# Kernel optimization log

Hardware: AMD Instinct MI355X
Metric: run time of the kernel (lower is better)

Reference implementation:

```python
import jax, jax.numpy as jnp
import numpy as np

# Static module configuration (matches init_kwargs)
H, W, C, K = 40, 40, 1, 5
HOUT, WOUT = H - K + 1, W - K + 1
P = HOUT * WOUT * C          # patch_count = 1296
L = K * K * C                # patch_length = 25
M = 384                      # num_inducing
N = 64                       # batch
JITTER = 1e-6


def extract_patches(X):
    """im2col: [N,H,W,C] -> [N, P, L], stride 1, VALID."""
    i = jnp.arange(HOUT)[:, None] + jnp.arange(K)[None, :]   # [HOUT,K]
    j = jnp.arange(WOUT)[:, None] + jnp.arange(K)[None, :]   # [WOUT,K]
    p = X[:, i, :, :]            # [N,HOUT,K,W,C]
    p = p[:, :, :, j, :]         # [N,HOUT,K,WOUT,K,C]
    p = jnp.transpose(p, (0, 1, 3, 2, 4, 5))  # [N,HOUT,WOUT,K,K,C]
    return p.reshape(X.shape[0], P, L)


def rbf(A, B, var, ls):
    """Isotropic RBF kernel K(A,B), A:[a,L], B:[b,L] -> [a,b]."""
    a2 = jnp.sum(A * A, -1)[:, None]
    b2 = jnp.sum(B * B, -1)[None, :]
    sq = jnp.maximum(a2 + b2 - 2.0 * (A @ B.T), 0.0)
    return var * jnp.exp(-0.5 * sq / (ls * ls))


def setup_inputs() -> dict:
    key = jax.random.key(0)
    k0, k1, k2, k3 = jax.random.split(key, 4)
    X = jax.random.normal(k0, (N, H * W * C), jnp.float32)
    Z = jax.random.normal(k1, (M, L), jnp.float32)
    q_mu = jax.random.normal(k2, (M, 1), jnp.float32)
    q_sqrt = jax.random.normal(k3, (M, M), jnp.float32) * 0.1
    variance = jnp.ones((1,), jnp.float32)
    lengthscale = jnp.ones((1,), jnp.float32) * 2.0
    return {"X": X, "Z": Z, "q_mu": q_mu, "q_sqrt": q_sqrt,
            "variance": variance, "lengthscale": lengthscale}


def reference(X, Z, q_mu, q_sqrt, variance, lengthscale):
    """conditional_ND with full_cov=False, white=False, Zero mean function.
    Returns (mean [N,P], var [N,P])."""
    var = variance[0]
    ls = lengthscale[0]
    n = X.shape[0]
    Ximg = X.reshape(n, H, W, C)
    patches = extract_patches(Ximg)                       # [N,P,L]

    # Kuf: M x (N*P) -- same as reshaping PMN_Kzx; solves act on M only
    Kuf = rbf(Z, patches.reshape(n * P, L), var, ls)       # [M, N*P]
    Kuu = rbf(Z, Z, var, ls) + JITTER * jnp.eye(M, dtype=X.dtype)
    Lu = jnp.linalg.cholesky(Kuu)

    # A = Kuu^{-1} Kuf via two triangular solves (white=False path)
    A = jax.scipy.linalg.solve_triangular(Lu, Kuf, lower=True)
    A = jax.scipy.linalg.solve_triangular(Lu.T, A, lower=False)
    A = A.reshape(M, n, P)                                 # [M,N,P]

    # mean = A^T q_mu per patch (q_mu shared across patches), + Zero mean fn
    mean = jnp.einsum('mnp,m->np', A, q_mu[:, 0])          # [N,P]

    # S - Kuu, shared across all P outputs
    Lq = jnp.tril(q_sqrt)
    SK = Lq @ Lq.T - Kuu                                   # [M,M]

    # diag of A^T (S - Kuu) A per (n,p)
    diag = jnp.einsum('mnp,mk,knp->np', A, SK, A)          # [N,P]

    # Kdiag of RBF kernel is the variance
    Kdiag = var * jnp.ones((n, P), X.dtype)
    return mean, Kdiag + diag
```

## Files before the change

kernel.cpp:

```cpp
#include <hip/hip_runtime.h>
#include <hip/hip_bf16.h>

#define HH 40
#define WW 40
#define KK 5
#define PP 1296
#define LL 25
#define MM 384
#define NN 64
#define NPTS (NN * PP)
#define JITTER 1e-6f

typedef unsigned short u16;
typedef unsigned int   u32;
using short8  = __attribute__((ext_vector_type(8))) short;
using floatx4 = __attribute__((ext_vector_type(4))) float;

#define FRAG_N (MM * MM)
#define ZFRAG_N (24 * 64 * 8)

__device__ inline u16 f2bf(float v) {
    u32 b = __float_as_uint(v);
    return (u16)((b + 0x7FFFu + ((b >> 16) & 1u)) >> 16);
}
__device__ inline float bf2f(u16 h) { return __uint_as_float(((u32)h) << 16); }
__device__ inline void split_bf16(float v, u16& hi, u16& lo) {
    hi = f2bf(v);
    lo = f2bf(v - bf2f(hi));
}

__device__ inline int frag_idx(int m, int k) {
    return (((m >> 4) * 12 + (k >> 5)) * 64 + ((m & 15) + (((k >> 3) & 3) << 4))) * 8 + (k & 7);
}

__device__ inline void frag_gemm64(const u16* __restrict__ Ah, const u16* __restrict__ Al,
                                   const u16* __restrict__ Bh, const u16* __restrict__ Bl,
                                   int bi, int bj, int w, int l, floatx4 acc[2][2]) {
    int mt0 = bi * 4 + 2 * (w & 1);
    int nt0 = bj * 4 + 2 * (w >> 1);
#pragma unroll
    for (int i = 0; i < 2; ++i)
#pragma unroll
        for (int jn = 0; jn < 2; ++jn) { floatx4 z = {0.f, 0.f, 0.f, 0.f}; acc[i][jn] = z; }
    for (int kt = 0; kt < 12; ++kt) {
        int ab0 = (((mt0 + 0) * 12 + kt) * 64 + l) * 8;
        int ab1 = (((mt0 + 1) * 12 + kt) * 64 + l) * 8;
        int bb0 = (((nt0 + 0) * 12 + kt) * 64 + l) * 8;
        int bb1 = (((nt0 + 1) * 12 + kt) * 64 + l) * 8;
        short8 a0h = *(const short8*)&Ah[ab0];
        short8 a0l = *(const short8*)&Al[ab0];
        short8 a1h = *(const short8*)&Ah[ab1];
        short8 a1l = *(const short8*)&Al[ab1];
        short8 b0h = *(const short8*)&Bh[bb0];
        short8 b0l = *(const short8*)&Bl[bb0];
        short8 b1h = *(const short8*)&Bh[bb1];
        short8 b1l = *(const short8*)&Bl[bb1];
        acc[0][0] = __builtin_amdgcn_mfma_f32_16x16x32_bf16(a0h, b0h, acc[0][0], 0, 0, 0);
        acc[0][0] = __builtin_amdgcn_mfma_f32_16x16x32_bf16(a0h, b0l, acc[0][0], 0, 0, 0);
        acc[0][0] = __builtin_amdgcn_mfma_f32_16x16x32_bf16(a0l, b0h, acc[0][0], 0, 0, 0);
        acc[0][1] = __builtin_amdgcn_mfma_f32_16x16x32_bf16(a0h, b1h, acc[0][1], 0, 0, 0);
        acc[0][1] = __builtin_amdgcn_mfma_f32_16x16x32_bf16(a0h, b1l, acc[0][1], 0, 0, 0);
        acc[0][1] = __builtin_amdgcn_mfma_f32_16x16x32_bf16(a0l, b1h, acc[0][1], 0, 0, 0);
        acc[1][0] = __builtin_amdgcn_mfma_f32_16x16x32_bf16(a1h, b0h, acc[1][0], 0, 0, 0);
        acc[1][0] = __builtin_amdgcn_mfma_f32_16x16x32_bf16(a1h, b0l, acc[1][0], 0, 0, 0);
        acc[1][0] = __builtin_amdgcn_mfma_f32_16x16x32_bf16(a1l, b0h, acc[1][0], 0, 0, 0);
        acc[1][1] = __builtin_amdgcn_mfma_f32_16x16x32_bf16(a1h, b1h, acc[1][1], 0, 0, 0);
        acc[1][1] = __builtin_amdgcn_mfma_f32_16x16x32_bf16(a1h, b1l, acc[1][1], 0, 0, 0);
        acc[1][1] = __builtin_amdgcn_mfma_f32_16x16x32_bf16(a1l, b1h, acc[1][1], 0, 0, 0);
    }
}

__device__ inline void dwrite_frag(u16* __restrict__ Oh, u16* __restrict__ Ol,
                                   int m, int p, float v) {
    int idx = frag_idx(m, p);
    u16 hi, lo;
    split_bf16(v, hi, lo);
    Oh[idx] = hi; Ol[idx] = lo;
}

__device__ inline void load_r0(const float* __restrict__ Kuu, float alpha,
                               int row, int kt, int l, short8& h8, short8& l8) {
    int kb = kt * 32 + ((l >> 4) << 3);
    const float* p = &Kuu[row * MM + kb];
    float4 f0 = *(const float4*)p;
    float4 f1 = *(const float4*)(p + 4);
    float vv[8] = {f0.x, f0.y, f0.z, f0.w, f1.x, f1.y, f1.z, f1.w};
#pragma unroll
    for (int j = 0; j < 8; ++j) {
        float r = ((row == kb + j) ? 1.f : 0.f) - alpha * vv[j];
        u16 h, lo;
        split_bf16(r, h, lo);
        h8[j] = (short)h; l8[j] = (short)lo;
    }
}

__global__ void __launch_bounds__(384) prep_kernel(
    const float* __restrict__ Z, const float* __restrict__ q_sqrt,
    const float* __restrict__ var_p, const float* __restrict__ ls_p,
    float* __restrict__ Kuu, float* __restrict__ rsum, float* __restrict__ z2g,
    u16* __restrict__ Qh, u16* __restrict__ Ql,
    u16* __restrict__ Zfh, u16* __restrict__ Zfl) {
    __shared__ float Zs[LL];
    __shared__ float red[384];
    int r = blockIdx.x, tid = threadIdx.x;
    if (tid < LL) Zs[tid] = Z[r * LL + tid];
    __syncthreads();
    float var = var_p[0];
    float ls = ls_p[0];
    float c0 = -0.5f / (ls * ls);
    float s = 0.f;
#pragma unroll
    for (int d = 0; d < LL; ++d) {
        float dd = Zs[d] - Z[tid * LL + d];
        s += dd * dd;
    }
    float v = var * expf(c0 * s);
    if (tid == r) v += JITTER;
    Kuu[r * MM + tid] = v;
    red[tid] = v;
    __syncthreads();
    if (tid < 128) red[tid] += red[tid + 256];
    __syncthreads();
    for (int o = 128; o > 0; o >>= 1) {
        if (tid < o) red[tid] += red[tid + o];
        __syncthreads();
    }
    if (tid == 0) {
        rsum[r] = red[0];
        float t = 0.f;
#pragma unroll
        for (int d = 0; d < LL; ++d) t += Zs[d] * Zs[d];
        z2g[r] = t;
    }
    {
        int o = r * MM + tid;
        int j = o & 7, ln = (o >> 3) & 63, kt = (o >> 9) % 12, mt = o / 6144;
        int m = mt * 16 + (ln & 15);
        int k = kt * 32 + ((ln >> 4) << 3) + j;
        float qv = (k <= m) ? q_sqrt[m * MM + k] : 0.f;
        u16 h, lo;
        split_bf16(qv, h, lo);
        Qh[o] = h; Ql[o] = lo;
        if (o < ZFRAG_N) {
            int zt = o >> 9;
            int mz = zt * 16 + (ln & 15);
            int kd = ((ln >> 4) << 3) + j;
            float zv = (kd < LL) ? Z[mz * LL + kd] : 0.f;
            split_bf16(zv, h, lo);
            Zfh[o] = h; Zfl[o] = lo;
        }
    }
}

__global__ void __launch_bounds__(256) ns1_kernel(
    const float* __restrict__ Kuu, const float* __restrict__ rsum,
    const u16* __restrict__ Qh, const u16* __restrict__ Ql,
    u16* __restrict__ Xh, u16* __restrict__ Xl,
    u16* __restrict__ Rh, u16* __restrict__ Rl,
    u16* __restrict__ SKh, u16* __restrict__ SKl) {
    __shared__ float red[256];
    int tid = threadIdx.x, blk = blockIdx.x;
    int w = tid >> 6, l = tid & 63;
    float alpha = 0.f;
    if (blk < 72) {
        float v0 = rsum[tid];
        if (tid < 128) v0 = fmaxf(v0, rsum[tid + 256]);
        red[tid] = v0;
        __syncthreads();
        for (int o = 128; o > 0; o >>= 1) {
            if (tid < o) red[tid] = fmaxf(red[tid], red[tid + o]);
            __syncthreads();
        }
        alpha = 1.0f / red[0];
    }
    if (blk < 36) {
        float a2 = alpha * alpha;
        for (int o = blk * 256 + tid; o < FRAG_N; o += 36 * 256) {
            int j = o & 7, ln = (o >> 3) & 63, kt = (o >> 9) % 12, mt = o / 6144;
            int m = mt * 16 + (ln & 15);
            int k = kt * 32 + ((ln >> 4) << 3) + j;
            float v = ((m == k) ? 2.f * alpha : 0.f) - a2 * Kuu[m * MM + k];
            u16 h, lo;
            split_bf16(v, h, lo);
            Xh[o] = h; Xl[o] = lo;
        }
    } else if (blk < 72) {
        int tile = blk - 36;
        int bi = tile / 6, bj = tile % 6;
        int mt0 = bi * 4 + 2 * (w & 1), nt0 = bj * 4 + 2 * (w >> 1);
        floatx4 acc[2][2];
#pragma unroll
        for (int i = 0; i < 2; ++i)
#pragma unroll
            for (int jn = 0; jn < 2; ++jn) { floatx4 z = {0.f,0.f,0.f,0.f}; acc[i][jn] = z; }
        for (int kt = 0; kt < 12; ++kt) {
            short8 a0h, a0l, a1h, a1l, b0h, b0l, b1h, b1l;
            load_r0(Kuu, alpha, (mt0 + 0) * 16 + (l & 15), kt, l, a0h, a0l);
            load_r0(Kuu, alpha, (mt0 + 1) * 16 + (l & 15), kt, l, a1h, a1l);
            load_r0(Kuu, alpha, (nt0 + 0) * 16 + (l & 15), kt, l, b0h, b0l);
            load_r0(Kuu, alpha, (nt0 + 1) * 16 + (l & 15), kt, l, b1h, b1l);
            acc[0][0] = __builtin_amdgcn_mfma_f32_16x16x32_bf16(a0h, b0h, acc[0][0], 0, 0, 0);
            acc[0][0] = __builtin_amdgcn_mfma_f32_16x16x32_bf16(a0h, b0l, acc[0][0], 0, 0, 0);
            acc[0][0] = __builtin_amdgcn_mfma_f32_16x16x32_bf16(a0l, b0h, acc[0][0], 0, 0, 0);
            acc[0][1] = __builtin_amdgcn_mfma_f32_16x16x32_bf16(a0h, b1h, acc[0][1], 0, 0, 0);
            acc[0][1] = __builtin_amdgcn_mfma_f32_16x16x32_bf16(a0h, b1l, acc[0][1], 0, 0, 0);
            acc[0][1] = __builtin_amdgcn_mfma_f32_16x16x32_bf16(a0l, b1h, acc[0][1], 0, 0, 0);
            acc[1][0] = __builtin_amdgcn_mfma_f32_16x16x32_bf16(a1h, b0h, acc[1][0], 0, 0, 0);
            acc[1][0] = __builtin_amdgcn_mfma_f32_16x16x32_bf16(a1h, b0l, acc[1][0], 0, 0, 0);
            acc[1][0] = __builtin_amdgcn_mfma_f32_16x16x32_bf16(a1l, b0h, acc[1][0], 0, 0, 0);
            acc[1][1] = __builtin_amdgcn_mfma_f32_16x16x32_bf16(a1h, b1h, acc[1][1], 0, 0, 0);
            acc[1][1] = __builtin_amdgcn_mfma_f32_16x16x32_bf16(a1h, b1l, acc[1][1], 0, 0, 0);
            acc[1][1] = __builtin_amdgcn_mfma_f32_16x16x32_bf16(a1l, b1h, acc[1][1], 0, 0, 0);
        }
#pragma unroll
        for (int i = 0; i < 2; ++i)
#pragma unroll
            for (int jn = 0; jn < 2; ++jn)
#pragma unroll
                for (int j = 0; j < 4; ++j) {
                    int m = (mt0 + i) * 16 + ((l >> 4) << 2) + j;
                    int p = (nt0 + jn) * 16 + (l & 15);
                    dwrite_frag(Rh, Rl, m, p, acc[i][jn][j]);
                }
    } else {
        int tile = blk - 72;
        int bi = tile / 6, bj = tile % 6;
        floatx4 acc[2][2];
        frag_gemm64(Qh, Ql, Qh, Ql, bi, bj, w, l, acc);
        int mt0 = bi * 4 + 2 * (w & 1), nt0 = bj * 4 + 2 * (w >> 1);
#pragma unroll
        for (int i = 0; i < 2; ++i)
#pragma unroll
            for (int jn = 0; jn < 2; ++jn)
#pragma unroll
                for (int j = 0; j < 4; ++j) {
                    int m = (mt0 + i) * 16 + ((l >> 4) << 2) + j;
                    int p = (nt0 + jn) * 16 + (l & 15);
                    dwrite_frag(SKh, SKl, m, p, acc[i][jn][j] - Kuu[m * MM + p]);
                }
    }
}

__global__ void __launch_bounds__(256) ns_kernel(
    const u16* __restrict__ cxh, const u16* __restrict__ cxl,
    const u16* __restrict__ crh, const u16* __restrict__ crl,
    u16* __restrict__ nxh, u16* __restrict__ nxl,
    u16* __restrict__ nrh, u16* __restrict__ nrl) {
    int blk = blockIdx.x, tid = threadIdx.x;
    bool isX = (blk < 36);
    int tile = isX ? blk : blk - 36;
    int bi = tile / 6, bj = tile % 6;
    int w = tid >> 6, l = tid & 63;
    floatx4 acc[2][2];
    frag_gemm64(isX ? cxh : crh, isX ? cxl : crl, crh, crl, bi, bj, w, l, acc);
    int mt0 = bi * 4 + 2 * (w & 1), nt0 = bj * 4 + 2 * (w >> 1);
    u16* Oh = isX ? nxh : nrh;
    u16* Ol = isX ? nxl : nrl;
#pragma unroll
    for (int i = 0; i < 2; ++i)
#pragma unroll
        for (int jn = 0; jn < 2; ++jn)
#pragma unroll
            for (int j = 0; j < 4; ++j) {
                int m = (mt0 + i) * 16 + ((l >> 4) << 2) + j;
                int p = (nt0 + jn) * 16 + (l & 15);
                float v = acc[i][jn][j];
                if (isX) {
                    int id = frag_idx(m, p);
                    v += bf2f(cxh[id]) + bf2f(cxl[id]);
                }
                dwrite_frag(Oh, Ol, m, p, v);
            }
}

__global__ void __launch_bounds__(256) y_kernel(
    const u16* __restrict__ Xh, const u16* __restrict__ Xl,
    const u16* __restrict__ SKh, const u16* __restrict__ SKl,
    const float* __restrict__ qmu,
    u16* __restrict__ Yh, u16* __restrict__ Yl, float* __restrict__ cvec) {
    __shared__ float q[MM];
    int tid = threadIdx.x, blk = blockIdx.x;
    int w = tid >> 6, l = tid & 63;
    if (blk < 36) {
        int bi = blk / 6, bj = blk % 6;
        floatx4 acc[2][2];
        frag_gemm64(Xh, Xl, SKh, SKl, bi, bj, w, l, acc);
        int mt0 = bi * 4 + 2 * (w & 1), nt0 = bj * 4 + 2 * (w >> 1);
#pragma unroll
        for (int i = 0; i < 2; ++i)
#pragma unroll
            for (int jn = 0; jn < 2; ++jn)
#pragma unroll
                for (int j = 0; j < 4; ++j) {
                    int m = (mt0 + i) * 16 + ((l >> 4) << 2) + j;
                    int p = (nt0 + jn) * 16 + (l & 15);
                    dwrite_frag(Yh, Yl, m, p, acc[i][jn][j]);
                }
    } else {
        if (tid < MM) q[tid] = qmu[tid];
        if (tid + 256 < MM) q[tid + 256] = qmu[tid + 256];
        __syncthreads();
        int mt = (blk - 36) * 4 + w;
        float s = 0.f;
        for (int kt = 0; kt < 12; ++kt) {
            int b = ((mt * 12 + kt) * 64 + l) * 8;
            short8 h8 = *(const short8*)&Xh[b];
            short8 l8 = *(const short8*)&Xl[b];
            int kb = kt * 32 + ((l >> 4) << 3);
#pragma unroll
            for (int j = 0; j < 8; ++j)
                s += (bf2f((u16)h8[j]) + bf2f((u16)l8[j])) * q[kb + j];
        }
        s += __shfl_xor(s, 16);
        s += __shfl_xor(s, 32);
        if (l < 16) cvec[mt * 16 + l] = s;
    }
}

__global__ void __launch_bounds__(256) bq_kernel(
    const u16* __restrict__ Yh, const u16* __restrict__ Yl,
    const u16* __restrict__ Xh, const u16* __restrict__ Xl,
    u16* __restrict__ Bh, u16* __restrict__ Bl) {
    int blk = blockIdx.x, tid = threadIdx.x;
    int bi = blk / 6, bj = blk % 6;
    int w = tid >> 6, l = tid & 63;
    floatx4 acc[2][2];
    frag_gemm64(Yh, Yl, Xh, Xl, bi, bj, w, l, acc);
    int mt0 = bi * 4 + 2 * (w & 1), nt0 = bj * 4 + 2 * (w >> 1);
#pragma unroll
    for (int i = 0; i < 2; ++i)
#pragma unroll
        for (int jn = 0; jn < 2; ++jn)
#pragma unroll
            for (int j = 0; j < 4; ++j) {
                int m = (mt0 + i) * 16 + ((l >> 4) << 2) + j;
                int p = (nt0 + jn) * 16 + (l & 15);
                dwrite_frag(Bh, Bl, m, p, acc[i][jn][j]);
            }
}

__global__ void __launch_bounds__(512) main_kernel(
    const float* __restrict__ Xin,
    const u16* __restrict__ Zfh, const u16* __restrict__ Zfl,
    const float* __restrict__ z2g,
    const u16* __restrict__ Bfh, const u16* __restrict__ Bfl,
    const float* __restrict__ cvec,
    const float* __restrict__ var_p, const float* __restrict__ ls_p,
    float* __restrict__ out) {
    __shared__ u16 kh[12 * 8 * 64 * 8];
    __shared__ float patch[128 * 36];
    __shared__ float zsq[MM];
    __shared__ float xsq[128];
    __shared__ float red[1024];

    int tid = threadIdx.x;
    int np0 = blockIdx.x * 128;
    float var = var_p[0];
    float ls = ls_p[0];
    float c2 = -0.72134752044f / (ls * ls);

    if (tid < MM) zsq[tid] = z2g[tid];
    for (int e = tid; e < 128 * 36; e += 512) {
        int pt = e / 36, c = e % 36;
        float v = 0.f;
        if (c < 25) {
            int np = np0 + pt;
            int n = np / PP, p = np % PP;
            int oi = p / 36, oj = p % 36;
            v = Xin[n * (HH * WW) + (oi + c / 5) * WW + (oj + c % 5)];
        }
        patch[e] = v;
    }
    __syncthreads();
    if (tid < 128) {
        float s = 0.f;
#pragma unroll
        for (int d = 0; d < LL; ++d) { float x = patch[tid * 36 + d]; s += x * x; }
        xsq[tid] = s;
    }
    __syncthreads();

    int w = tid >> 6, l = tid & 63;
    int u = l >> 4;

    u32 kpk[3][8][2];
    float mp[8] = {0.f, 0.f, 0.f, 0.f, 0.f, 0.f, 0.f, 0.f};

#pragma unroll
    for (int h = 0; h < 2; ++h) {
        short8 pbh[4], pbl[4];
#pragma unroll
        for (int nt = 0; nt < 4; ++nt) {
            int p = h * 64 + nt * 16 + (l & 15);
            int pb = p * 36 + (u << 3);
            float4 f0 = *(const float4*)&patch[pb];
            float4 f1 = *(const float4*)&patch[pb + 4];
            float xv[8] = {f0.x, f0.y, f0.z, f0.w, f1.x, f1.y, f1.z, f1.w};
#pragma unroll
            for (int j = 0; j < 8; ++j) {
                u16 hh, lo;
                split_bf16(xv[j], hh, lo);
                pbh[nt][j] = (short)hh;
                pbl[nt][j] = (short)lo;
            }
        }
        floatx4 acc2[3][4];
#pragma unroll
        for (int i = 0; i < 3; ++i) {
            int zt = w * 3 + i;
            short8 zah = *(const short8*)&Zfh[(zt * 64 + l) * 8];
            short8 zal = *(const short8*)&Zfl[(zt * 64 + l) * 8];
#pragma unroll
            for (int nt = 0; nt < 4; ++nt) {
                floatx4 z = {0.f, 0.f, 0.f, 0.f};
                z = __builtin_amdgcn_mfma_f32_16x16x32_bf16(zah, pbh[nt], z, 0, 0, 0);
                z = __builtin_amdgcn_mfma_f32_16x16x32_bf16(zah, pbl[nt], z, 0, 0, 0);
                z = __builtin_amdgcn_mfma_f32_16x16x32_bf16(zal, pbh[nt], z, 0, 0, 0);
                acc2[i][nt] = z;
            }
        }
#pragma unroll
        for (int i = 0; i < 3; ++i) {
            int a2 = w * 3 + i;
            int kt = a2 >> 1;
            int rr = 2 * (a2 & 1) + (u >> 1);
            int k0 = a2 * 16 + 4 * u;
            float4 c4 = *(const float4*)&cvec[k0];
            float cvl[4] = {c4.x, c4.y, c4.z, c4.w};
#pragma unroll
            for (int nt = 0; nt < 4; ++nt) {
                int ntg = h * 4 + nt;
                int p = h * 64 + nt * 16 + (l & 15);
                u16 hi[4];
#pragma unroll
                for (int j = 0; j < 4; ++j) {
                    float s = zsq[k0 + j] + xsq[p] - 2.f * acc2[i][nt][j];
                    float v = var * exp2f(s * c2);
                    mp[ntg] += cvl[j] * v;
                    hi[j] = f2bf(v);
                }
                u32 p0 = (u32)hi[0] | ((u32)hi[1] << 16);
                u32 p1 = (u32)hi[2] | ((u32)hi[3] << 16);
                int base = ((kt * 8 + ntg) * 64 + rr * 16 + (l & 15)) * 8 + 4 * (u & 1);
                *(u32*)&kh[base]     = p0;
                *(u32*)&kh[base + 2] = p1;
                kpk[i][ntg][0] = p0;
                kpk[i][ntg][1] = p1;
            }
        }
    }

#pragma unroll
    for (int nt = 0; nt < 8; ++nt) {
        mp[nt] += __shfl_xor(mp[nt], 16);
        mp[nt] += __shfl_xor(mp[nt], 32);
    }
    if (l < 16) {
#pragma unroll
        for (int nt = 0; nt < 8; ++nt) red[w * 128 + nt * 16 + l] = mp[nt];
    }
    __syncthreads();
    if (tid < 128) {
        float s = 0.f;
#pragma unroll
        for (int ww = 0; ww < 8; ++ww) s += red[ww * 128 + tid];
        out[np0 + tid] = s;
    }

    floatx4 acc[3][8];
#pragma unroll
    for (int i = 0; i < 3; ++i)
#pragma unroll
        for (int nt = 0; nt < 8; ++nt) { floatx4 z = {0.f, 0.f, 0.f, 0.f}; acc[i][nt] = z; }
    for (int kt = 0; kt < 12; ++kt) {
        short8 bh[8];
#pragma unroll
        for (int nt = 0; nt < 8; ++nt)
            bh[nt] = *(const short8*)&kh[((kt * 8 + nt) * 64 + l) * 8];
#pragma unroll
        for (int i = 0; i < 3; ++i) {
            int mt = w * 3 + i;
            int ab = ((mt * 12 + kt) * 64 + l) * 8;
            short8 ah = *(const short8*)&Bfh[ab];
            short8 al = *(const short8*)&Bfl[ab];
#pragma unroll
            for (int nt = 0; nt < 8; ++nt) {
                acc[i][nt] = __builtin_amdgcn_mfma_f32_16x16x32_bf16(ah, bh[nt], acc[i][nt], 0, 0, 0);
                acc[i][nt] = __builtin_amdgcn_mfma_f32_16x16x32_bf16(al, bh[nt], acc[i][nt], 0, 0, 0);
            }
        }
    }
    __syncthreads();

    float dp[8] = {0.f, 0.f, 0.f, 0.f, 0.f, 0.f, 0.f, 0.f};
#pragma unroll
    for (int i = 0; i < 3; ++i)
#pragma unroll
        for (int nt = 0; nt < 8; ++nt) {
            float kv0 = bf2f((u16)(kpk[i][nt][0] & 0xFFFFu));
            float kv1 = bf2f((u16)(kpk[i][nt][0] >> 16));
            float kv2 = bf2f((u16)(kpk[i][nt][1] & 0xFFFFu));
            float kv3 = bf2f((u16)(kpk[i][nt][1] >> 16));
            dp[nt] += kv0 * acc[i][nt][0] + kv1 * acc[i][nt][1]
                    + kv2 * acc[i][nt][2] + kv3 * acc[i][nt][3];
        }
#pragma unroll
    for (int nt = 0; nt < 8; ++nt) {
        dp[nt] += __shfl_xor(dp[nt], 16);
        dp[nt] += __shfl_xor(dp[nt], 32);
    }
    if (l < 16) {
#pragma unroll
        for (int nt = 0; nt < 8; ++nt) red[w * 128 + nt * 16 + l] = dp[nt];
    }
    __syncthreads();
    if (tid < 128) {
        float s = 0.f;
#pragma unroll
        for (int ww = 0; ww < 8; ++ww) s += red[ww * 128 + tid];
        out[NPTS + np0 + tid] = var + s;
    }
}

extern "C" void kernel_launch(void* const* d_in, const int* in_sizes, int n_in,
                              void* d_out, int out_size, void* d_ws, size_t ws_size,
                              hipStream_t stream) {
    const float* Xin    = (const float*)d_in[0];
    const float* Z      = (const float*)d_in[1];
    const float* q_mu   = (const float*)d_in[2];
    const float* q_sqrt = (const float*)d_in[3];
    const float* var_p  = (const float*)d_in[4];
    const float* ls_p   = (const float*)d_in[5];
    float* out = (float*)d_out;

    const size_t HB = (size_t)FRAG_N * 2;
    char* base = (char*)d_ws;
    float* Kuu = (float*)base;
    u16* Bqh = (u16*)base;
    u16* Bql = (u16*)(base + HB);
    u16* Xh_a = (u16*)(base + 2 * HB);
    u16* Xl_a = (u16*)(base + 3 * HB);
    u16* Xh_b = (u16*)(base + 4 * HB);
    u16* Xl_b = (u16*)(base + 5 * HB);
    u16* Rh_a = (u16*)(base + 6 * HB);
    u16* Rl_a = (u16*)(base + 7 * HB);
    u16* Rh_b = (u16*)(base + 8 * HB);
    u16* Rl_b = (u16*)(base + 9 * HB);
    u16* Qh   = (u16*)(base + 10 * HB);
    u16* Ql   = (u16*)(base + 11 * HB);
    u16* Yh = Qh;
    u16* Yl = Ql;
    u16* SKh  = (u16*)(base + 12 * HB);
    u16* SKl  = (u16*)(base + 13 * HB);
    char* pF = base + 14 * HB;
    u16* Zfh = (u16*)pF;
    u16* Zfl = (u16*)(pF + ZFRAG_N * 2);
    float* z2g  = (float*)(pF + ZFRAG_N * 4);
    float* cvec = z2g + MM;
    float* rsum = cvec + MM;

    prep_kernel<<<MM, 384, 0, stream>>>(Z, q_sqrt, var_p, ls_p, Kuu, rsum, z2g,
                                        Qh, Ql, Zfh, Zfl);
    ns1_kernel<<<108, 256, 0, stream>>>(Kuu, rsum, Qh, Ql,
                                        Xh_b, Xl_b, Rh_b, Rl_b, SKh, SKl);
    u16 *cxh = Xh_b, *cxl = Xl_b, *nxh = Xh_a, *nxl = Xl_a;
    u16 *crh = Rh_b, *crl = Rl_b, *nrh = Rh_a, *nrl = Rl_a;
    for (int it = 0; it < 5; ++it) {
        ns_kernel<<<72, 256, 0, stream>>>(cxh, cxl, crh, crl, nxh, nxl, nrh, nrl);
        u16* t;
        t = cxh; cxh = nxh; nxh = t;
        t = cxl; cxl = nxl; nxl = t;
        t = crh; crh = nrh; nrh = t;
        t = crl; crl = nrl; nrl = t;
    }
    y_kernel<<<42, 256, 0, stream>>>(cxh, cxl, SKh, SKl, q_mu, Yh, Yl, cvec);
    bq_kernel<<<36, 256, 0, stream>>>(Yh, Yl, cxh, cxl, Bqh, Bql);
    main_kernel<<<NPTS / 128, 512, 0, stream>>>(Xin, Zfh, Zfl, z2g, Bqh, Bql, cvec,
                                                var_p, ls_p, out);
}
```

Measured before the change: 197.2 us.

## Precompute Kuu fragments in prep and split main kernel into two interleaved halves

Prep now also writes Kuu in bf16 hi/lo fragment layout, computed directly from Z. ns1 can then run its R0 GEMM through the shared frag_gemm64 helper on K·K and apply the alpha-scaled identity terms in the epilogue, instead of converting Kuu on the fly. The main kernel is restructured so the B·K GEMM for the first 64 patches runs before the second half's kernel evaluation, with the mean reduction moved to the end. This is meant to overlap work and cut register pressure from holding 8 bh tiles at once, but it adds a __syncthreads, recomputes Kuu entries per element in prep (25-dim loop), and changes the rounding of the R0 algebra.

```diff
diff --git a/kernel.cpp b/kernel.cpp
--- a/kernel.cpp
+++ b/kernel.cpp
@@ -78,26 +78,11 @@
     Oh[idx] = hi; Ol[idx] = lo;
 }
 
-__device__ inline void load_r0(const float* __restrict__ Kuu, float alpha,
-                               int row, int kt, int l, short8& h8, short8& l8) {
-    int kb = kt * 32 + ((l >> 4) << 3);
-    const float* p = &Kuu[row * MM + kb];
-    float4 f0 = *(const float4*)p;
-    float4 f1 = *(const float4*)(p + 4);
-    float vv[8] = {f0.x, f0.y, f0.z, f0.w, f1.x, f1.y, f1.z, f1.w};
-#pragma unroll
-    for (int j = 0; j < 8; ++j) {
-        float r = ((row == kb + j) ? 1.f : 0.f) - alpha * vv[j];
-        u16 h, lo;
-        split_bf16(r, h, lo);
-        h8[j] = (short)h; l8[j] = (short)lo;
-    }
-}
-
 __global__ void __launch_bounds__(384) prep_kernel(
     const float* __restrict__ Z, const float* __restrict__ q_sqrt,
     const float* __restrict__ var_p, const float* __restrict__ ls_p,
     float* __restrict__ Kuu, float* __restrict__ rsum, float* __restrict__ z2g,
+    u16* __restrict__ Kfh, u16* __restrict__ Kfl,
     u16* __restrict__ Qh, u16* __restrict__ Ql,
     u16* __restrict__ Zfh, u16* __restrict__ Zfl) {
     __shared__ float Zs[LL];
@@ -137,10 +122,20 @@
         int j = o & 7, ln = (o >> 3) & 63, kt = (o >> 9) % 12, mt = o / 6144;
         int m = mt * 16 + (ln & 15);
         int k = kt * 32 + ((ln >> 4) << 3) + j;
+        u16 h, lo;
         float qv = (k <= m) ? q_sqrt[m * MM + k] : 0.f;
-        u16 h, lo;
         split_bf16(qv, h, lo);
         Qh[o] = h; Ql[o] = lo;
+        float s2 = 0.f;
+#pragma unroll
+        for (int d = 0; d < LL; ++d) {
+            float dd = Z[m * LL + d] - Z[k * LL + d];
+            s2 += dd * dd;
+        }
+        float kv = var * expf(c0 * s2);
+        if (m == k) kv += JITTER;
+        split_bf16(kv, h, lo);
+        Kfh[o] = h; Kfl[o] = lo;
         if (o < ZFRAG_N) {
             int zt = o >> 9;
             int mz = zt * 16 + (ln & 15);
@@ -154,6 +149,7 @@
 
 __global__ void __launch_bounds__(256) ns1_kernel(
     const float* __restrict__ Kuu, const float* __restrict__ rsum,
+    const u16* __restrict__ Kfh, const u16* __restrict__ Kfl,
     const u16* __restrict__ Qh, const u16* __restrict__ Ql,
     u16* __restrict__ Xh, u16* __restrict__ Xl,
     u16* __restrict__ Rh, u16* __restrict__ Rl,
@@ -187,31 +183,10 @@
     } else if (blk < 72) {
         int tile = blk - 36;
         int bi = tile / 6, bj = tile % 6;
+        floatx4 acc[2][2];
+        frag_gemm64(Kfh, Kfl, Kfh, Kfl, bi, bj, w, l, acc);
         int mt0 = bi * 4 + 2 * (w & 1), nt0 = bj * 4 + 2 * (w >> 1);
-        floatx4 acc[2][2];
-#pragma unroll
-        for (int i = 0; i < 2; ++i)
-#pragma unroll
-            for (int jn = 0; jn < 2; ++jn) { floatx4 z = {0.f,0.f,0.f,0.f}; acc[i][jn] = z; }
-        for (int kt = 0; kt < 12; ++kt) {
-            short8 a0h, a0l, a1h, a1l, b0h, b0l, b1h, b1l;
-            load_r0(Kuu, alpha, (mt0 + 0) * 16 + (l & 15), kt, l, a0h, a0l);
-            load_r0(Kuu, alpha, (mt0 + 1) * 16 + (l & 15), kt, l, a1h, a1l);
-            load_r0(Kuu, alpha, (nt0 + 0) * 16 + (l & 15), kt, l, b0h, b0l);
-            load_r0(Kuu, alpha, (nt0 + 1) * 16 + (l & 15), kt, l, b1h, b1l);
-            acc[0][0] = __builtin_amdgcn_mfma_f32_16x16x32_bf16(a0h, b0h, acc[0][0], 0, 0, 0);
-            acc[0][0] = __builtin_amdgcn_mfma_f32_16x16x32_bf16(a0h, b0l, acc[0][0], 0, 0, 0);
-            acc[0][0] = __builtin_amdgcn_mfma_f32_16x16x32_bf16(a0l, b0h, acc[0][0], 0, 0, 0);
-            acc[0][1] = __builtin_amdgcn_mfma_f32_16x16x32_bf16(a0h, b1h, acc[0][1], 0, 0, 0);
-            acc[0][1] = __builtin_amdgcn_mfma_f32_16x16x32_bf16(a0h, b1l, acc[0][1], 0, 0, 0);
-            acc[0][1] = __builtin_amdgcn_mfma_f32_16x16x32_bf16(a0l, b1h, acc[0][1], 0, 0, 0);
-            acc[1][0] = __builtin_amdgcn_mfma_f32_16x16x32_bf16(a1h, b0h, acc[1][0], 0, 0, 0);
-            acc[1][0] = __builtin_amdgcn_mfma_f32_16x16x32_bf16(a1h, b0l, acc[1][0], 0, 0, 0);
-            acc[1][0] = __builtin_amdgcn_mfma_f32_16x16x32_bf16(a1l, b0h, acc[1][0], 0, 0, 0);
-            acc[1][1] = __builtin_amdgcn_mfma_f32_16x16x32_bf16(a1h, b1h, acc[1][1], 0, 0, 0);
-            acc[1][1] = __builtin_amdgcn_mfma_f32_16x16x32_bf16(a1h, b1l, acc[1][1], 0, 0, 0);
-            acc[1][1] = __builtin_amdgcn_mfma_f32_16x16x32_bf16(a1l, b1h, acc[1][1], 0, 0, 0);
-        }
+        float a2 = alpha * alpha;
 #pragma unroll
         for (int i = 0; i < 2; ++i)
 #pragma unroll
@@ -220,7 +195,9 @@
                 for (int j = 0; j < 4; ++j) {
                     int m = (mt0 + i) * 16 + ((l >> 4) << 2) + j;
                     int p = (nt0 + jn) * 16 + (l & 15);
-                    dwrite_frag(Rh, Rl, m, p, acc[i][jn][j]);
+                    float v = a2 * acc[i][jn][j] - 2.f * alpha * Kuu[m * MM + p]
+                            + ((m == p) ? 1.f : 0.f);
+                    dwrite_frag(Rh, Rl, m, p, v);
                 }
     } else {
         int tile = blk - 72;
@@ -386,24 +363,23 @@
     u32 kpk[3][8][2];
     float mp[8] = {0.f, 0.f, 0.f, 0.f, 0.f, 0.f, 0.f, 0.f};
 
-#pragma unroll
-    for (int h = 0; h < 2; ++h) {
-        short8 pbh[4], pbl[4];
-#pragma unroll
-        for (int nt = 0; nt < 4; ++nt) {
-            int p = h * 64 + nt * 16 + (l & 15);
-            int pb = p * 36 + (u << 3);
-            float4 f0 = *(const float4*)&patch[pb];
-            float4 f1 = *(const float4*)&patch[pb + 4];
-            float xv[8] = {f0.x, f0.y, f0.z, f0.w, f1.x, f1.y, f1.z, f1.w};
-#pragma unroll
-            for (int j = 0; j < 8; ++j) {
-                u16 hh, lo;
-                split_bf16(xv[j], hh, lo);
-                pbh[nt][j] = (short)hh;
-                pbl[nt][j] = (short)lo;
-            }
-        }
+    short8 pb0h[4], pb0l[4];
+#pragma unroll
+    for (int nt = 0; nt < 4; ++nt) {
+        int p = nt * 16 + (l & 15);
+        int pb = p * 36 + (u << 3);
+        float4 f0 = *(const float4*)&patch[pb];
+        float4 f1 = *(const float4*)&patch[pb + 4];
+        float xv[8] = {f0.x, f0.y, f0.z, f0.w, f1.x, f1.y, f1.z, f1.w};
+#pragma unroll
+        for (int j = 0; j < 8; ++j) {
+            u16 hh, lo;
+            split_bf16(xv[j], hh, lo);
+            pb0h[nt][j] = (short)hh;
+            pb0l[nt][j] = (short)lo;
+        }
+    }
+    {
         floatx4 acc2[3][4];
 #pragma unroll
         for (int i = 0; i < 3; ++i) {
@@ -413,9 +389,9 @@
 #pragma unroll
             for (int nt = 0; nt < 4; ++nt) {
                 floatx4 z = {0.f, 0.f, 0.f, 0.f};
-                z = __builtin_amdgcn_mfma_f32_16x16x32_bf16(zah, pbh[nt], z, 0, 0, 0);
-                z = __builtin_amdgcn_mfma_f32_16x16x32_bf16(zah, pbl[nt], z, 0, 0, 0);
-                z = __builtin_amdgcn_mfma_f32_16x16x32_bf16(zal, pbh[nt], z, 0, 0, 0);
+                z = __builtin_amdgcn_mfma_f32_16x16x32_bf16(zah, pb0h[nt], z, 0, 0, 0);
+                z = __builtin_amdgcn_mfma_f32_16x16x32_bf16(zah, pb0l[nt], z, 0, 0, 0);
+                z = __builtin_amdgcn_mfma_f32_16x16x32_bf16(zal, pb0h[nt], z, 0, 0, 0);
                 acc2[i][nt] = z;
             }
         }
@@ -429,8 +405,96 @@
             float cvl[4] = {c4.x, c4.y, c4.z, c4.w};
 #pragma unroll
             for (int nt = 0; nt < 4; ++nt) {
-                int ntg = h * 4 + nt;
-                int p = h * 64 + nt * 16 + (l & 15);
+                int p = nt * 16 + (l & 15);
+                u16 hi[4];
+#pragma unroll
+                for (int j = 0; j < 4; ++j) {
+                    float s = zsq[k0 + j] + xsq[p] - 2.f * acc2[i][nt][j];
+                    float v = var * exp2f(s * c2);
+                    mp[nt] += cvl[j] * v;
+                    hi[j] = f2bf(v);
+                }
+                u32 p0 = (u32)hi[0] | ((u32)hi[1] << 16);
+                u32 p1 = (u32)hi[2] | ((u32)hi[3] << 16);
+                int base = ((kt * 8 + nt) * 64 + rr * 16 + (l & 15)) * 8 + 4 * (u & 1);
+                *(u32*)&kh[base]     = p0;
+                *(u32*)&kh[base + 2] = p1;
+                kpk[i][nt][0] = p0;
+                kpk[i][nt][1] = p1;
+            }
+        }
+    }
+    short8 pb1h[4], pb1l[4];
+#pragma unroll
+    for (int nt = 0; nt < 4; ++nt) {
+        int p = 64 + nt * 16 + (l & 15);
+        int pb = p * 36 + (u << 3);
+        float4 f0 = *(const float4*)&patch[pb];
+        float4 f1 = *(const float4*)&patch[pb + 4];
+        float xv[8] = {f0.x, f0.y, f0.z, f0.w, f1.x, f1.y, f1.z, f1.w};
+#pragma unroll
+        for (int j = 0; j < 8; ++j) {
+            u16 hh, lo;
+            split_bf16(xv[j], hh, lo);
+            pb1h[nt][j] = (short)hh;
+            pb1l[nt][j] = (short)lo;
+        }
+    }
+    __syncthreads();
+
+    floatx4 acc[3][8];
+#pragma unroll
+    for (int i = 0; i < 3; ++i)
+#pragma unroll
+        for (int nt = 0; nt < 8; ++nt) { floatx4 z = {0.f, 0.f, 0.f, 0.f}; acc[i][nt] = z; }
+
+    for (int kt = 0; kt < 12; ++kt) {
+        short8 bh[4];
+#pragma unroll
+        for (int nt = 0; nt < 4; ++nt)
+            bh[nt] = *(const short8*)&kh[((kt * 8 + nt) * 64 + l) * 8];
+#pragma unroll
+        for (int i = 0; i < 3; ++i) {
+            int mt = w * 3 + i;
+            int ab = ((mt * 12 + kt) * 64 + l) * 8;
+            short8 ah = *(const short8*)&Bfh[ab];
+            short8 al = *(const short8*)&Bfl[ab];
+#pragma unroll
+            for (int nt = 0; nt < 4; ++nt) {
+                acc[i][nt] = __builtin_amdgcn_mfma_f32_16x16x32_bf16(ah, bh[nt], acc[i][nt], 0, 0, 0);
+                acc[i][nt] = __builtin_amdgcn_mfma_f32_16x16x32_bf16(al, bh[nt], acc[i][nt], 0, 0, 0);
+            }
+        }
+    }
+
+    {
+        floatx4 acc2[3][4];
+#pragma unroll
+        for (int i = 0; i < 3; ++i) {
+            int zt = w * 3 + i;
+            short8 zah = *(const short8*)&Zfh[(zt * 64 + l) * 8];
+            short8 zal = *(const short8*)&Zfl[(zt * 64 + l) * 8];
+#pragma unroll
+            for (int nt = 0; nt < 4; ++nt) {
+                floatx4 z = {0.f, 0.f, 0.f, 0.f};
+                z = __builtin_amdgcn_mfma_f32_16x16x32_bf16(zah, pb1h[nt], z, 0, 0, 0);
+                z = __builtin_amdgcn_mfma_f32_16x16x32_bf16(zah, pb1l[nt], z, 0, 0, 0);
+                z = __builtin_amdgcn_mfma_f32_16x16x32_bf16(zal, pb1h[nt], z, 0, 0, 0);
+                acc2[i][nt] = z;
+            }
+        }
+#pragma unroll
+        for (int i = 0; i < 3; ++i) {
+            int a2 = w * 3 + i;
+            int kt = a2 >> 1;
+            int rr = 2 * (a2 & 1) + (u >> 1);
+            int k0 = a2 * 16 + 4 * u;
+            float4 c4 = *(const float4*)&cvec[k0];
+            float cvl[4] = {c4.x, c4.y, c4.z, c4.w};
+#pragma unroll
+            for (int nt = 0; nt < 4; ++nt) {
+                int ntg = 4 + nt;
+                int p = 64 + nt * 16 + (l & 15);
                 u16 hi[4];
 #pragma unroll
                 for (int j = 0; j < 4; ++j) {
@@ -449,34 +513,13 @@
             }
         }
     }
-
-#pragma unroll
-    for (int nt = 0; nt < 8; ++nt) {
-        mp[nt] += __shfl_xor(mp[nt], 16);
-        mp[nt] += __shfl_xor(mp[nt], 32);
-    }
-    if (l < 16) {
-#pragma unroll
-        for (int nt = 0; nt < 8; ++nt) red[w * 128 + nt * 16 + l] = mp[nt];
-    }
-    __syncthreads();
-    if (tid < 128) {
-        float s = 0.f;
-#pragma unroll
-        for (int ww = 0; ww < 8; ++ww) s += red[ww * 128 + tid];
-        out[np0 + tid] = s;
-    }
-
-    floatx4 acc[3][8];
-#pragma unroll
-    for (int i = 0; i < 3; ++i)
-#pragma unroll
-        for (int nt = 0; nt < 8; ++nt) { floatx4 z = {0.f, 0.f, 0.f, 0.f}; acc[i][nt] = z; }
+    __syncthreads();
+
     for (int kt = 0; kt < 12; ++kt) {
-        short8 bh[8];
-#pragma unroll
-        for (int nt = 0; nt < 8; ++nt)
-            bh[nt] = *(const short8*)&kh[((kt * 8 + nt) * 64 + l) * 8];
+        short8 bh[4];
+#pragma unroll
+        for (int nt = 0; nt < 4; ++nt)
+            bh[nt] = *(const short8*)&kh[((kt * 8 + 4 + nt) * 64 + l) * 8];
 #pragma unroll
         for (int i = 0; i < 3; ++i) {
             int mt = w * 3 + i;
@@ -484,14 +527,30 @@
             short8 ah = *(const short8*)&Bfh[ab];
             short8 al = *(const short8*)&Bfl[ab];
 #pragma unroll
-            for (int nt = 0; nt < 8; ++nt) {
-                acc[i][nt] = __builtin_amdgcn_mfma_f32_16x16x32_bf16(ah, bh[nt], acc[i][nt], 0, 0, 0);
-                acc[i][nt] = __builtin_amdgcn_mfma_f32_16x16x32_bf16(al, bh[nt], acc[i][nt], 0, 0, 0);
-            }
-        }
-    }
-    __syncthreads();
-
+            for (int nt = 0; nt < 4; ++nt) {
+                acc[i][4 + nt] = __builtin_amdgcn_mfma_f32_16x16x32_bf16(ah, bh[nt], acc[i][4 + nt], 0, 0, 0);
+                acc[i][4 + nt] = __builtin_amdgcn_mfma_f32_16x16x32_bf16(al, bh[nt], acc[i][4 + nt], 0, 0, 0);
+            }
+        }
+    }
+
+#pragma unroll
+    for (int nt = 0; nt < 8; ++nt) {
+        mp[nt] += __shfl_xor(mp[nt], 16);
+        mp[nt] += __shfl_xor(mp[nt], 32);
+    }
+    if (l < 16) {
+#pragma unroll
+        for (int nt = 0; nt < 8; ++nt) red[w * 128 + nt * 16 + l] = mp[nt];
+    }
+    __syncthreads();
+    if (tid < 128) {
+        float s = 0.f;
+#pragma unroll
+        for (int ww = 0; ww < 8; ++ww) s += red[ww * 128 + tid];
+        out[np0 + tid] = s;
+    }
+    __syncthreads();
     float dp[8] = {0.f, 0.f, 0.f, 0.f, 0.f, 0.f, 0.f, 0.f};
 #pragma unroll
     for (int i = 0; i < 3; ++i)
@@ -540,6 +599,8 @@
     u16* Bql = (u16*)(base + HB);
     u16* Xh_a = (u16*)(base + 2 * HB);
     u16* Xl_a = (u16*)(base + 3 * HB);
+    u16* Kfh = Xh_a;
+    u16* Kfl = Xl_a;
     u16* Xh_b = (u16*)(base + 4 * HB);
     u16* Xl_b = (u16*)(base + 5 * HB);
     u16* Rh_a = (u16*)(base + 6 * HB);
@@ -560,8 +621,8 @@
     float* rsum = cvec + MM;
 
     prep_kernel<<<MM, 384, 0, stream>>>(Z, q_sqrt, var_p, ls_p, Kuu, rsum, z2g,
-                                        Qh, Ql, Zfh, Zfl);
-    ns1_kernel<<<108, 256, 0, stream>>>(Kuu, rsum, Qh, Ql,
+                                        Kfh, Kfl, Qh, Ql, Zfh, Zfl);
+    ns1_kernel<<<108, 256, 0, stream>>>(Kuu, rsum, Kfh, Kfl, Qh, Ql,
                                         Xh_b, Xl_b, Rh_b, Rl_b, SKh, SKl);
     u16 *cxh = Xh_b, *cxl = Xl_b, *nxh = Xh_a, *nxl = Xl_a;
     u16 *crh = Rh_b, *crl = Rl_b, *nrh = Rh_a, *nrl = Rl_a;
```

Result: slower. 267.0 us (+35.4%).
